# Kernel tuning notes

Measured on AMD Instinct MI355X. Metric: run time of the kernel, lower is better.

## Reference

```python
import jax, jax.numpy as jnp
import numpy as np

S, B, H2, V = 2048, 16, 2048, 1024  # seq, batch, 2*hidden_dim, v_dim
ALPHA_S = 0.5


def setup_inputs() -> dict:
    key = jax.random.key(0)
    ks = jax.random.split(key, 8)
    sc_in = 1.0 / np.sqrt(H2)
    sc_v = 1.0 / np.sqrt(V)
    return {
        "hidden": jax.random.normal(ks[0], (S, B, H2), dtype=jnp.float32),
        "z": jax.random.normal(ks[1], (S, B, H2), dtype=jnp.float32),
        "Ww": jax.random.normal(ks[2], (H2, V), dtype=jnp.float32) * sc_in,
        "bw": jax.random.normal(ks[3], (V,), dtype=jnp.float32) * sc_in,
        "Wz": jax.random.normal(ks[4], (H2, V), dtype=jnp.float32) * sc_in,
        "bz": jax.random.normal(ks[5], (V,), dtype=jnp.float32) * sc_in,
        "Vw": jax.random.normal(ks[6], (V, 1), dtype=jnp.float32) * sc_v,
        "vb": jax.random.normal(ks[7], (1,), dtype=jnp.float32) * sc_v,
        "w_a": jnp.zeros((), dtype=jnp.float32),
    }


def reference(hidden, z, Ww, bw, Wz, bz, Vw, vb, w_a):
    # sum_w = w_w(hidden) + w_z(z) + w_a * alpha_s   -> [S, B, V]
    sum_w = (jnp.einsum("sbh,hv->sbv", hidden, Ww) + bw
             + jnp.einsum("sbh,hv->sbv", z, Wz) + bz
             + w_a * ALPHA_S)
    # u = v(tanh(sum_w))                              -> [S, B, 1]
    u = jnp.einsum("sbv,vo->sbo", jnp.tanh(sum_w), Vw) + vb
    # softmax over the sequence (dim 0)
    attention = jax.nn.softmax(u, axis=0)
    return attention
```

## Files before the change

kernel.cpp:

```cpp
#include <hip/hip_runtime.h>
#include <hip/hip_bf16.h>
#include <stdint.h>

#define S_DIM 2048
#define B_DIM 16
#define H2_DIM 2048
#define V_DIM 1024
#define M_DIM (S_DIM * B_DIM)
#define K_HALF 2048
#define K_TOT 4096

typedef __attribute__((ext_vector_type(8))) short s16x8;
typedef __attribute__((ext_vector_type(4))) float f32x4;

__device__ __forceinline__ uint16_t f2bf(float f) {
    union { float f; uint32_t u; } c; c.f = f;
    uint32_t u = c.u;
    u += 0x7fffu + ((u >> 16) & 1u);
    return (uint16_t)(u >> 16);
}

__device__ __forceinline__ uint32_t pack_bf16_rn(float a, float b) {
    union { float f; uint32_t u; } ca, cb; ca.f = a; cb.f = b;
    uint32_t ua = ca.u + 0x8000u;
    uint32_t ub = cb.u + 0x8000u;
    return __builtin_amdgcn_perm(ub, ua, 0x07060302u);
}

__device__ __forceinline__ float fast_tanh(float x) {
    float e = __expf(2.0f * x);
    return 1.0f - 2.0f / (e + 1.0f);
}

__device__ __forceinline__ void gload_lds16(const void* g, void* l) {
    __builtin_amdgcn_global_load_lds(
        (__attribute__((address_space(1))) void*)(uintptr_t)g,
        (__attribute__((address_space(3))) void*)(uint32_t)(uintptr_t)l,
        16, 0, 0);
}

__global__ void transposeB(const float* __restrict__ Ww, const float* __restrict__ Wz,
                           uint16_t* __restrict__ B1, uint16_t* __restrict__ B2) {
    __shared__ float tile[32][33];
    const float* src = blockIdx.z ? Wz : Ww;
    uint16_t* dst = blockIdx.z ? B2 : B1;
    int k0 = blockIdx.x * 32, v0 = blockIdx.y * 32;
    int tv = threadIdx.x & 31, tk = threadIdx.x >> 5;
#pragma unroll
    for (int r = 0; r < 4; r++) {
        int k = tk * 4 + r;
        tile[k][tv] = src[(size_t)(k0 + k) * V_DIM + v0 + tv];
    }
    __syncthreads();
#pragma unroll
    for (int r = 0; r < 4; r++) {
        int v = tk * 4 + r;
        dst[(size_t)(v0 + v) * K_HALF + k0 + tv] = f2bf(tile[tv][v]);
    }
}

__global__ __launch_bounds__(256, 2) void gemm_kernel(
    const float* __restrict__ F1, const float* __restrict__ F2,
    const uint16_t* __restrict__ B1, const uint16_t* __restrict__ B2,
    const float* __restrict__ bw, const float* __restrict__ bz,
    const float* __restrict__ wa_p, const float* __restrict__ Vw,
    float* __restrict__ u) {
    __shared__ __align__(16) uint16_t lA[128 * 64];
    __shared__ __align__(16) uint16_t lB[2][256 * 64];

    const int tid = threadIdx.x;
    const int lane = tid & 63;
    const int wv = tid >> 6;
    const int wm = (wv >> 1) * 64, wn = (wv & 1) * 128;
    const int id = blockIdx.x;
    const int nBase = ((id >> 3) & 3) * 256;
    const int mBase = ((id & 7) + ((id >> 5) << 3)) * 128;
    const int lr = lane >> 3;
    const int lc = lane & 7;
    const int cg = lc ^ lr;
    const int col = lane & 15, quad = lane >> 4;

    f32x4 acc[4][8] = {};

    const float* aRow[2];
    const uint16_t* bRow[2];
    {
        const size_t aoff = (size_t)(mBase + wv * 32 + lr) * K_HALF + cg * 8;
        aRow[0] = F1 + aoff; aRow[1] = F2 + aoff;
        const size_t boff = (size_t)(nBase + wv * 64 + lr) * K_HALF + cg * 8;
        bRow[0] = B1 + boff; bRow[1] = B2 + boff;
    }

    float4 ar[4][2];

    auto loadA = [&](int kb) {
        const float* base = aRow[kb >> 11] + (kb & (K_HALF - 1));
#pragma unroll
        for (int j = 0; j < 4; j++) {
            const float* gp = base + (size_t)(j * 8) * K_HALF;
            ar[j][0] = ((const float4*)gp)[0];
            ar[j][1] = ((const float4*)gp)[1];
        }
    };
    auto issueB = [&](int kb, int p) {
        const uint16_t* base = bRow[kb >> 11] + (kb & (K_HALF - 1));
#pragma unroll
        for (int j = 0; j < 8; j++)
            gload_lds16(base + (size_t)(j * 8) * K_HALF, &lB[p][(wv * 64 + j * 8) * 64]);
    };

    loadA(0);
    issueB(0, 0);

#pragma unroll 1
    for (int s = 0; s < 64; s++) {
        const int p = s & 1;

#pragma unroll
        for (int j = 0; j < 4; j++) {
            uint4 w = make_uint4(pack_bf16_rn(ar[j][0].x, ar[j][0].y),
                                 pack_bf16_rn(ar[j][0].z, ar[j][0].w),
                                 pack_bf16_rn(ar[j][1].x, ar[j][1].y),
                                 pack_bf16_rn(ar[j][1].z, ar[j][1].w));
            *(uint4*)&lA[(wv * 32 + j * 8 + lr) * 64 + lc * 8] = w;
        }

        if (s < 63) {
            const int kb2 = (s + 1) * 64;
            loadA(kb2);
            issueB(kb2, p ^ 1);
            asm volatile("s_waitcnt vmcnt(16) lgkmcnt(0)\n\ts_barrier" ::: "memory");
        } else {
            asm volatile("s_waitcnt vmcnt(0) lgkmcnt(0)\n\ts_barrier" ::: "memory");
        }

        const uint16_t* lb = lB[p];
#pragma unroll
        for (int kk = 0; kk < 2; kk++) {
            s16x8 af[4], bf[8];
            const int cidx = kk * 4 + quad;
#pragma unroll
            for (int i = 0; i < 4; i++) {
                int m = wm + i * 16 + col;
                af[i] = *(const s16x8*)&lA[m * 64 + ((cidx ^ (m & 7)) << 3)];
            }
#pragma unroll
            for (int j = 0; j < 8; j++) {
                int n = wn + j * 16 + col;
                bf[j] = *(const s16x8*)&lb[n * 64 + ((cidx ^ (n & 7)) << 3)];
            }
#pragma unroll
            for (int i = 0; i < 4; i++)
#pragma unroll
                for (int j = 0; j < 8; j++)
                    acc[i][j] = __builtin_amdgcn_mfma_f32_16x16x32_bf16(af[i], bf[j], acc[i][j], 0, 0, 0);
        }
        asm volatile("s_barrier" ::: "memory");
    }

    const float wa05 = wa_p[0] * 0.5f;
    float biasv[8], vwv[8];
#pragma unroll
    for (int j = 0; j < 8; j++) {
        int n = nBase + wn + j * 16 + col;
        biasv[j] = bw[n] + bz[n] + wa05;
        vwv[j] = Vw[n];
    }
#pragma unroll
    for (int i = 0; i < 4; i++) {
#pragma unroll
        for (int r = 0; r < 4; r++) {
            float sv = 0.f;
#pragma unroll
            for (int j = 0; j < 8; j++) {
                float xv = acc[i][j][r] + biasv[j];
                sv += fast_tanh(xv) * vwv[j];
            }
            sv += __shfl_xor(sv, 8);
            sv += __shfl_xor(sv, 4);
            sv += __shfl_xor(sv, 2);
            sv += __shfl_xor(sv, 1);
            if (col == 0)
                atomicAdd(&u[mBase + wm + i * 16 + quad * 4 + r], sv);
        }
    }
}

__global__ void softmax_kernel(float* __restrict__ u) {
    const int b = blockIdx.x;
    const int t = threadIdx.x;
    __shared__ float redm[4], reds[4];
    float v[8];
    float mx = -1e30f;
#pragma unroll
    for (int k = 0; k < 8; k++) {
        v[k] = u[(size_t)(t + k * 256) * B_DIM + b];
        mx = fmaxf(mx, v[k]);
    }
#pragma unroll
    for (int off = 32; off >= 1; off >>= 1) mx = fmaxf(mx, __shfl_xor(mx, off));
    if ((t & 63) == 0) redm[t >> 6] = mx;
    __syncthreads();
    mx = fmaxf(fmaxf(redm[0], redm[1]), fmaxf(redm[2], redm[3]));
    float s = 0.f;
#pragma unroll
    for (int k = 0; k < 8; k++) {
        v[k] = __expf(v[k] - mx);
        s += v[k];
    }
#pragma unroll
    for (int off = 32; off >= 1; off >>= 1) s += __shfl_xor(s, off);
    if ((t & 63) == 0) reds[t >> 6] = s;
    __syncthreads();
    s = reds[0] + reds[1] + reds[2] + reds[3];
    float inv = 1.0f / s;
#pragma unroll
    for (int k = 0; k < 8; k++)
        u[(size_t)(t + k * 256) * B_DIM + b] = v[k] * inv;
}

extern "C" void kernel_launch(void* const* d_in, const int* in_sizes, int n_in,
                              void* d_out, int out_size, void* d_ws, size_t ws_size,
                              hipStream_t stream) {
    const float* hidden = (const float*)d_in[0];
    const float* z = (const float*)d_in[1];
    const float* Ww = (const float*)d_in[2];
    const float* bw = (const float*)d_in[3];
    const float* Wz = (const float*)d_in[4];
    const float* bz = (const float*)d_in[5];
    const float* Vw = (const float*)d_in[6];
    const float* wa = (const float*)d_in[8];
    float* out = (float*)d_out;

    char* ws = (char*)d_ws;
    const size_t bBytes = (size_t)V_DIM * K_HALF * 2;
    uint16_t* wsB1 = (uint16_t*)ws;
    uint16_t* wsB2 = (uint16_t*)(ws + bBytes);

    hipMemsetAsync(d_out, 0, (size_t)M_DIM * sizeof(float), stream);

    transposeB<<<dim3(K_HALF / 32, V_DIM / 32, 2), 256, 0, stream>>>(Ww, Wz, wsB1, wsB2);

    gemm_kernel<<<dim3((M_DIM / 128) * (V_DIM / 256)), 256, 0, stream>>>(
        hidden, z, wsB1, wsB2, bw, bz, wa, Vw, out);

    softmax_kernel<<<B_DIM, 256, 0, stream>>>(out);
}
```

Measured before the change: 711.8 us.

## Load A operand straight into MFMA fragment registers, bypassing LDS

```diff
diff --git a/kernel.cpp b/kernel.cpp
--- a/kernel.cpp
+++ b/kernel.cpp
@@ -27,6 +27,13 @@
     return __builtin_amdgcn_perm(ub, ua, 0x07060302u);
 }
 
+__device__ __forceinline__ s16x8 pack8(float4 x, float4 y) {
+    union { uint4 u; s16x8 v; } r;
+    r.u = make_uint4(pack_bf16_rn(x.x, x.y), pack_bf16_rn(x.z, x.w),
+                     pack_bf16_rn(y.x, y.y), pack_bf16_rn(y.z, y.w));
+    return r.v;
+}
+
 __device__ __forceinline__ float fast_tanh(float x) {
     float e = __expf(2.0f * x);
     return 1.0f - 2.0f / (e + 1.0f);
@@ -65,7 +72,6 @@
     const float* __restrict__ bw, const float* __restrict__ bz,
     const float* __restrict__ wa_p, const float* __restrict__ Vw,
     float* __restrict__ u) {
-    __shared__ __align__(16) uint16_t lA[128 * 64];
     __shared__ __align__(16) uint16_t lB[2][256 * 64];
 
     const int tid = threadIdx.x;
@@ -81,26 +87,31 @@
     const int col = lane & 15, quad = lane >> 4;
 
     f32x4 acc[4][8] = {};
-
-    const float* aRow[2];
+    float4 ar[4][2][2];
+    s16x8 af[4][2];
+
+    uint32_t rowOff[4];
+#pragma unroll
+    for (int i = 0; i < 4; i++)
+        rowOff[i] = (uint32_t)((mBase + wm + i * 16 + col) * K_HALF + quad * 8);
+
     const uint16_t* bRow[2];
     {
-        const size_t aoff = (size_t)(mBase + wv * 32 + lr) * K_HALF + cg * 8;
-        aRow[0] = F1 + aoff; aRow[1] = F2 + aoff;
         const size_t boff = (size_t)(nBase + wv * 64 + lr) * K_HALF + cg * 8;
         bRow[0] = B1 + boff; bRow[1] = B2 + boff;
     }
 
-    float4 ar[4][2];
-
     auto loadA = [&](int kb) {
-        const float* base = aRow[kb >> 11] + (kb & (K_HALF - 1));
-#pragma unroll
-        for (int j = 0; j < 4; j++) {
-            const float* gp = base + (size_t)(j * 8) * K_HALF;
-            ar[j][0] = ((const float4*)gp)[0];
-            ar[j][1] = ((const float4*)gp)[1];
-        }
+        const float* Fh = (kb < K_HALF) ? F1 : F2;
+        const int kcol = kb & (K_HALF - 1);
+#pragma unroll
+        for (int i = 0; i < 4; i++)
+#pragma unroll
+            for (int kk = 0; kk < 2; kk++) {
+                const float* p = Fh + rowOff[i] + kcol + kk * 32;
+                ar[i][kk][0] = ((const float4*)p)[0];
+                ar[i][kk][1] = ((const float4*)p)[1];
+            }
     };
     auto issueB = [&](int kb, int p) {
         const uint16_t* base = bRow[kb >> 11] + (kb & (K_HALF - 1));
@@ -117,43 +128,32 @@
         const int p = s & 1;
 
 #pragma unroll
-        for (int j = 0; j < 4; j++) {
-            uint4 w = make_uint4(pack_bf16_rn(ar[j][0].x, ar[j][0].y),
-                                 pack_bf16_rn(ar[j][0].z, ar[j][0].w),
-                                 pack_bf16_rn(ar[j][1].x, ar[j][1].y),
-                                 pack_bf16_rn(ar[j][1].z, ar[j][1].w));
-            *(uint4*)&lA[(wv * 32 + j * 8 + lr) * 64 + lc * 8] = w;
-        }
+        for (int i = 0; i < 4; i++)
+#pragma unroll
+            for (int kk = 0; kk < 2; kk++)
+                af[i][kk] = pack8(ar[i][kk][0], ar[i][kk][1]);
 
         if (s < 63) {
             const int kb2 = (s + 1) * 64;
             loadA(kb2);
             issueB(kb2, p ^ 1);
-            asm volatile("s_waitcnt vmcnt(16) lgkmcnt(0)\n\ts_barrier" ::: "memory");
+            asm volatile("s_waitcnt vmcnt(24)\n\ts_barrier" ::: "memory");
         } else {
-            asm volatile("s_waitcnt vmcnt(0) lgkmcnt(0)\n\ts_barrier" ::: "memory");
+            asm volatile("s_waitcnt vmcnt(0)\n\ts_barrier" ::: "memory");
         }
 
         const uint16_t* lb = lB[p];
 #pragma unroll
         for (int kk = 0; kk < 2; kk++) {
-            s16x8 af[4], bf[8];
             const int cidx = kk * 4 + quad;
-#pragma unroll
-            for (int i = 0; i < 4; i++) {
-                int m = wm + i * 16 + col;
-                af[i] = *(const s16x8*)&lA[m * 64 + ((cidx ^ (m & 7)) << 3)];
-            }
 #pragma unroll
             for (int j = 0; j < 8; j++) {
                 int n = wn + j * 16 + col;
-                bf[j] = *(const s16x8*)&lb[n * 64 + ((cidx ^ (n & 7)) << 3)];
+                s16x8 b = *(const s16x8*)&lb[n * 64 + ((cidx ^ (n & 7)) << 3)];
+#pragma unroll
+                for (int i = 0; i < 4; i++)
+                    acc[i][j] = __builtin_amdgcn_mfma_f32_16x16x32_bf16(af[i][kk], b, acc[i][j], 0, 0, 0);
             }
-#pragma unroll
-            for (int i = 0; i < 4; i++)
-#pragma unroll
-                for (int j = 0; j < 8; j++)
-                    acc[i][j] = __builtin_amdgcn_mfma_f32_16x16x32_bf16(af[i], bf[j], acc[i][j], 0, 0, 0);
         }
         asm volatile("s_barrier" ::: "memory");
     }
```

Result: slower. 1.323 ms (+85.9%).
